# Optimization experiments

Hardware: AMD Instinct MI355X
Metric: run time of the kernel (lower is better)

The kernel has to match this reference:

```python
import jax, jax.numpy as jnp
import numpy as np

WAY = 5  # N_way from init


def setup_inputs() -> dict:
    key = jax.random.key(0)
    k1, k2, k3, k4 = jax.random.split(key, 4)
    N, c, h, w = 80, 2048, 16, 16
    S = 512  # shuffle_num
    x = jax.random.normal(k1, (N, c, h, w), dtype=jnp.float32)
    s_ca = jax.random.uniform(k2, (N, c, 1, 1), dtype=jnp.float32)
    # random channel indices per sample (stand-in for random.sample)
    rand_index = jax.random.randint(k3, (N, S), 0, c)
    # partner offset per sample (stand-in for random j != i)
    partner = jax.random.randint(k4, (N,), 0, N - 1)
    return {"x": x, "s_ca": s_ca, "rand_index": rand_index,
            "partner": partner, "shuffle_num": S}


def reference(x, s_ca, rand_index, partner, shuffle_num):
    N, c, h, w = x.shape
    way = WAY
    scores = s_ca.reshape(N, c)
    # per-sample top-k channels by attention score
    _, topk_idx = jax.lax.top_k(scores, shuffle_num)          # [N, S]
    # partner sample j != i (offset trick guarantees inequality)
    j = (jnp.arange(N) + 1 + partner) % N                      # [N]
    bi = jnp.arange(N)[:, None]                                # [N, 1]
    x_topk = x[bi, topk_idx]                                   # [N, S, h, w]
    x_part = x[j[:, None], rand_index]                         # [N, S, h, w]
    blend = 0.7 * x_topk + 0.3 * x_part
    # scatter blended channels back (batched gather-blend-scatter)
    aug_x = x.at[bi, topk_idx].set(blend)                      # [N, c, h, w]
    # group into (way, shot, ...) and concat original + augmented episodes
    x_r = x.reshape(way, -1, c, h, w)
    aug_r = aug_x.reshape(way, -1, c, h, w)
    out = jnp.concatenate((x_r, aug_r), axis=1)                # [way, 2*shot, c, h, w]
    s = s_ca.reshape(way, -1, c, 1, 1)
    s = jnp.concatenate((s, s), axis=1)                        # repeat(1,2,1,1,1)
    out = out * s
    return out.reshape(-1, c, h, w)                            # [2N, c, h, w]
```

## Files before the change

### kernel.cpp

```cpp
#include <hip/hip_runtime.h>

#define N_SAMP 80
#define C_CH   2048
#define HW     256
#define S_TOP  512
#define HW4    64

__global__ __launch_bounds__(256) void fused_shuffle_kernel(
    const float4* __restrict__ x4, const float* __restrict__ s_ca,
    const int* __restrict__ rand_index, const int* __restrict__ partner,
    float4* __restrict__ out4) {
  const unsigned int lane = threadIdx.x & 63u;
  const unsigned int pw = blockIdx.x * 4u + (threadIdx.x >> 6);
  const unsigned int n = pw >> 11;
  const unsigned int ch = pw & 2047u;
  const unsigned int g = n >> 4;
  const unsigned int b = n & 15u;

  const size_t out_plain =
      (((size_t)((g << 5) | b) * C_CH + ch) << 6) | lane;
  const size_t out_aug = out_plain + ((size_t)(16 * C_CH) << 6);

  const float* __restrict__ row = s_ca + (size_t)n * C_CH;
  const float si = row[ch];

  const float4 v = x4[((size_t)pw << 6) | lane];

  const float4* __restrict__ row4 = (const float4*)row;
  int cnt = 0;
#pragma unroll
  for (int q = 0; q < 8; ++q) {
    const float4 sv = row4[q * 64 + lane];
    const unsigned int j0 = 4u * (q * 64u + lane);
    cnt += __popcll(__ballot(sv.x > si || (sv.x == si && (j0 + 0u) < ch)));
    cnt += __popcll(__ballot(sv.y > si || (sv.y == si && (j0 + 1u) < ch)));
    cnt += __popcll(__ballot(sv.z > si || (sv.z == si && (j0 + 2u) < ch)));
    cnt += __popcll(__ballot(sv.w > si || (sv.w == si && (j0 + 3u) < ch)));
  }

  float4 pv = make_float4(v.x * si, v.y * si, v.z * si, v.w * si);
  float4 av = pv;

  if (cnt < S_TOP) {
    int jn = (int)n + 1 + partner[n];
    if (jn >= N_SAMP) jn -= N_SAMP;
    const int pc = rand_index[(size_t)n * S_TOP + cnt];
    const float4 u = x4[((((size_t)jn << 11) | (size_t)pc) << 6) | lane];
    av.x = (0.7f * v.x + 0.3f * u.x) * si;
    av.y = (0.7f * v.y + 0.3f * u.y) * si;
    av.z = (0.7f * v.z + 0.3f * u.z) * si;
    av.w = (0.7f * v.w + 0.3f * u.w) * si;
  }

  out4[out_plain] = pv;
  out4[out_aug] = av;
}

extern "C" void kernel_launch(void* const* d_in, const int* in_sizes, int n_in,
                              void* d_out, int out_size, void* d_ws,
                              size_t ws_size, hipStream_t stream) {
  const float* x = (const float*)d_in[0];
  const float* s_ca = (const float*)d_in[1];
  const int* rand_index = (const int*)d_in[2];
  const int* partner = (const int*)d_in[3];

  const int nblocks = (N_SAMP * C_CH) / 4;
  fused_shuffle_kernel<<<nblocks, 256, 0, stream>>>(
      (const float4*)x, s_ca, rand_index, partner, (float4*)d_out);
}
```

Measured before the change: 459.1 us.

## Process four channels per wavefront and rank with packed integer sort keys

After: 445.7 us. -2.9%, faster.

```diff
diff --git a/kernel.cpp b/kernel.cpp
--- a/kernel.cpp
+++ b/kernel.cpp
@@ -11,49 +11,77 @@
     const int* __restrict__ rand_index, const int* __restrict__ partner,
     float4* __restrict__ out4) {
   const unsigned int lane = threadIdx.x & 63u;
-  const unsigned int pw = blockIdx.x * 4u + (threadIdx.x >> 6);
-  const unsigned int n = pw >> 11;
-  const unsigned int ch = pw & 2047u;
+  const unsigned int wid = threadIdx.x >> 6;
+  const unsigned int blk = blockIdx.x;
+  const unsigned int n = blk >> 7;
+  const unsigned int ch0 = ((blk & 127u) << 4) | (wid << 2);
   const unsigned int g = n >> 4;
   const unsigned int b = n & 15u;
 
-  const size_t out_plain =
-      (((size_t)((g << 5) | b) * C_CH + ch) << 6) | lane;
-  const size_t out_aug = out_plain + ((size_t)(16 * C_CH) << 6);
+  const float* __restrict__ row = s_ca + (size_t)n * C_CH;
+  const float4* __restrict__ row4 = (const float4*)row;
 
-  const float* __restrict__ row = s_ca + (size_t)n * C_CH;
-  const float si = row[ch];
+  const float4 sq = row4[ch0 >> 2];
+  const float si[4] = {sq.x, sq.y, sq.z, sq.w};
 
-  const float4 v = x4[((size_t)pw << 6) | lane];
+  int jn = (int)n + 1 + partner[n];
+  if (jn >= N_SAMP) jn -= N_SAMP;
 
-  const float4* __restrict__ row4 = (const float4*)row;
-  int cnt = 0;
+  float4 v[4];
+#pragma unroll
+  for (int c = 0; c < 4; ++c)
+    v[c] = x4[(((size_t)n * C_CH + ch0 + c) << 6) | lane];
+
+  unsigned long long kc[4];
+#pragma unroll
+  for (int c = 0; c < 4; ++c) {
+    unsigned int bi = __float_as_uint(si[c]);
+    bi ^= (bi & 0x80000000u) ? 0xFFFFFFFFu : 0x80000000u;
+    kc[c] = ((unsigned long long)bi << 11) |
+            (unsigned long long)(C_CH - 1 - (ch0 + c));
+  }
+
+  int cnt[4] = {0, 0, 0, 0};
 #pragma unroll
   for (int q = 0; q < 8; ++q) {
     const float4 sv = row4[q * 64 + lane];
     const unsigned int j0 = 4u * (q * 64u + lane);
-    cnt += __popcll(__ballot(sv.x > si || (sv.x == si && (j0 + 0u) < ch)));
-    cnt += __popcll(__ballot(sv.y > si || (sv.y == si && (j0 + 1u) < ch)));
-    cnt += __popcll(__ballot(sv.z > si || (sv.z == si && (j0 + 2u) < ch)));
-    cnt += __popcll(__ballot(sv.w > si || (sv.w == si && (j0 + 3u) < ch)));
+    unsigned long long kj[4];
+#pragma unroll
+    for (int e = 0; e < 4; ++e) {
+      unsigned int bj = __float_as_uint((&sv.x)[e]);
+      bj ^= (bj & 0x80000000u) ? 0xFFFFFFFFu : 0x80000000u;
+      kj[e] = ((unsigned long long)bj << 11) |
+              (unsigned long long)(C_CH - 1 - (j0 + e));
+    }
+#pragma unroll
+    for (int c = 0; c < 4; ++c) {
+#pragma unroll
+      for (int e = 0; e < 4; ++e)
+        cnt[c] += __popcll(__ballot(kj[e] > kc[c]));
+    }
   }
 
-  float4 pv = make_float4(v.x * si, v.y * si, v.z * si, v.w * si);
-  float4 av = pv;
+  const size_t base_plain =
+      (((size_t)((g << 5) | b) * C_CH + ch0) << 6) | lane;
+  const size_t aug_off = ((size_t)(16 * C_CH)) << 6;
 
-  if (cnt < S_TOP) {
-    int jn = (int)n + 1 + partner[n];
-    if (jn >= N_SAMP) jn -= N_SAMP;
-    const int pc = rand_index[(size_t)n * S_TOP + cnt];
-    const float4 u = x4[((((size_t)jn << 11) | (size_t)pc) << 6) | lane];
-    av.x = (0.7f * v.x + 0.3f * u.x) * si;
-    av.y = (0.7f * v.y + 0.3f * u.y) * si;
-    av.z = (0.7f * v.z + 0.3f * u.z) * si;
-    av.w = (0.7f * v.w + 0.3f * u.w) * si;
+#pragma unroll
+  for (int c = 0; c < 4; ++c) {
+    const float s = si[c];
+    float4 pv = make_float4(v[c].x * s, v[c].y * s, v[c].z * s, v[c].w * s);
+    float4 av = pv;
+    if (cnt[c] < S_TOP) {
+      const int pc = rand_index[(size_t)n * S_TOP + cnt[c]];
+      const float4 u = x4[((((size_t)jn << 11) | (size_t)pc) << 6) | lane];
+      av.x = (0.7f * v[c].x + 0.3f * u.x) * s;
+      av.y = (0.7f * v[c].y + 0.3f * u.y) * s;
+      av.z = (0.7f * v[c].z + 0.3f * u.z) * s;
+      av.w = (0.7f * v[c].w + 0.3f * u.w) * s;
+    }
+    out4[base_plain + ((size_t)c << 6)] = pv;
+    out4[base_plain + aug_off + ((size_t)c << 6)] = av;
   }
-
-  out4[out_plain] = pv;
-  out4[out_aug] = av;
 }
 
 extern "C" void kernel_launch(void* const* d_in, const int* in_sizes, int n_in,
@@ -64,7 +92,7 @@
   const int* rand_index = (const int*)d_in[2];
   const int* partner = (const int*)d_in[3];
 
-  const int nblocks = (N_SAMP * C_CH) / 4;
+  const int nblocks = (N_SAMP * C_CH) / 16;
   fused_shuffle_kernel<<<nblocks, 256, 0, stream>>>(
       (const float4*)x, s_ca, rand_index, partner, (float4*)d_out);
 }
```
